# Optimization experiments

Hardware: AMD Instinct MI355X
Metric: run time of the kernel (lower is better)

Reference implementation:

```python
import jax, jax.numpy as jnp
import numpy as np

B_, N, C, H = 2048, 49, 384, 12
WH, WW = 7, 7
HEAD_DIM = C // H
SCALE = HEAD_DIM ** -0.5
TABLE = (2 * WH - 1) * (2 * WW - 1)  # 169


def _relative_position_index():
    coords = np.stack(np.meshgrid(np.arange(WH), np.arange(WW), indexing='ij'))  # [2,Wh,Ww]
    flat = coords.reshape(2, -1)  # [2,N]
    rel = flat[:, :, None] - flat[:, None, :]  # [2,N,N]
    rel = rel.transpose(1, 2, 0).astype(np.int32)  # [N,N,2]
    rel[:, :, 0] += WH - 1
    rel[:, :, 1] += WW - 1
    rel[:, :, 0] *= 2 * WW - 1
    return rel.sum(-1)  # [N,N] int32 in [0,169)


def setup_inputs() -> dict:
    key = jax.random.key(0)
    ks = jax.random.split(key, 8)
    return {
        'x': jax.random.normal(ks[0], (B_, N, C), jnp.float32),
        'mask': jax.random.normal(ks[1], (B_, 1, N, N), jnp.float32),
        'stagein': jax.random.uniform(ks[2], (B_, N, C), jnp.float32),
        'rel_bias_table': jax.random.normal(ks[3], (TABLE, H), jnp.float32) * 0.02,
        'rel_pos_index': jnp.asarray(_relative_position_index()),
        'qkv_w': jax.random.normal(ks[4], (3 * C, C), jnp.float32) * 0.02,
        'qkv_b': jax.random.normal(ks[5], (3 * C,), jnp.float32) * 0.02,
        'proj_w': jax.random.normal(ks[6], (C, C), jnp.float32) * 0.02,
        'proj_b': jax.random.normal(ks[7], (C,), jnp.float32) * 0.02,
    }


def reference(x, mask, stagein, rel_bias_table, rel_pos_index, qkv_w, qkv_b, proj_w, proj_b):
    x = x * stagein  # stagein is not None branch
    qkv = x @ qkv_w.T + qkv_b  # [B_, N, 3C]
    qkv = qkv.reshape(B_, N, 3, H, HEAD_DIM).transpose(2, 0, 3, 1, 4)  # [3,B_,H,N,hd]
    q, k, v = qkv[0], qkv[1], qkv[2]
    q = q * SCALE
    attn = jnp.einsum('bhnd,bhmd->bhnm', q, k)  # [B_,H,N,N]
    # relative position bias gather: [N*N] -> [N,N,H] -> [1,H,N,N]
    bias = rel_bias_table[rel_pos_index.reshape(-1)].reshape(N, N, H)
    bias = bias.transpose(2, 0, 1)[None]
    attn = jax.nn.softmax(attn + bias + mask, axis=-1)
    out = jnp.einsum('bhnm,bhmd->bhnd', attn, v)  # [B_,H,N,hd]
    out = out.transpose(0, 2, 1, 3).reshape(B_, N, C)
    return out @ proj_w.T + proj_b
```

## Files before the change

kernel.cpp:

```cpp
#include <hip/hip_runtime.h>
#include <hip/hip_bf16.h>
#include <stdint.h>

#define NWIN 2048
#define NTOK 49
#define CDIM 384
#define NHEAD 12
#define HD 32
#define C3 1152
#define NN2 2401
#define MROWS 100352

typedef __bf16 bf16x8 __attribute__((ext_vector_type(8)));
typedef float f32x4 __attribute__((ext_vector_type(4)));
typedef uint32_t u32x4 __attribute__((ext_vector_type(4)));
typedef unsigned int u32;

static __device__ __forceinline__ unsigned short f2bf(float f) {
  uint32_t u = __builtin_bit_cast(uint32_t, f);
  u += 0x7fffu + ((u >> 16) & 1u);
  return (unsigned short)(u >> 16);
}

static __device__ __forceinline__ u32 pk2(float a, float b) {
  return (u32)f2bf(a) | ((u32)f2bf(b) << 16);
}

static __device__ __forceinline__ void gload_lds16(const void* g, void* l) {
  __builtin_amdgcn_global_load_lds((const __attribute__((address_space(1))) void*)g,
                                   (__attribute__((address_space(3))) void*)l,
                                   16, 0, 0);
}

static __device__ __forceinline__ bf16x8 zero8() {
  u32x4 z = {0u, 0u, 0u, 0u};
  return __builtin_bit_cast(bf16x8, z);
}

__global__ void prep_kernel(const float* __restrict__ qkv_w, const float* __restrict__ proj_w,
                            const float* __restrict__ table, const int* __restrict__ idx,
                            unsigned short* __restrict__ wq, unsigned short* __restrict__ wp,
                            float* __restrict__ biasT) {
  const int NW1 = C3 * CDIM;
  const int NW2 = CDIM * CDIM;
  const int NB = NHEAD * NN2;
  int i = blockIdx.x * blockDim.x + threadIdx.x;
  int stride = gridDim.x * blockDim.x;
  for (int t = i; t < NW1 + NW2 + NB; t += stride) {
    if (t < NW1) {
      wq[t] = f2bf(qkv_w[t]);
    } else if (t < NW1 + NW2) {
      int j = t - NW1;
      wp[j] = f2bf(proj_w[j]);
    } else {
      int j = t - NW1 - NW2;
      int h = j / NN2;
      int nm = j - h * NN2;
      int m = nm / 49, n = nm - m * 49;
      biasT[j] = table[idx[n * 49 + m] * NHEAD + h];
    }
  }
}

__global__ void maskT_kernel(const float* __restrict__ mask, float* __restrict__ maskT) {
  __shared__ float t[NN2];
  const int b = blockIdx.x;
  for (int i = threadIdx.x; i < NN2; i += 256) t[i] = mask[(size_t)b * NN2 + i];
  __syncthreads();
  for (int i = threadIdx.x; i < NN2; i += 256) {
    int m = i / 49, n = i - m * 49;
    maskT[(size_t)b * NN2 + i] = t[n * 49 + m];
  }
}

__global__ void mul_kernel(const float4* __restrict__ x, const float4* __restrict__ s,
                           u32x4* __restrict__ A, int n8) {
  int i0 = blockIdx.x * blockDim.x + threadIdx.x;
  int stride = gridDim.x * blockDim.x;
  for (int t = i0; t < n8; t += stride) {
    float4 a0 = x[2 * t], a1 = x[2 * t + 1];
    float4 b0 = s[2 * t], b1 = s[2 * t + 1];
    union { unsigned short us[8]; u32x4 v; } o;
    o.us[0] = f2bf(a0.x * b0.x); o.us[1] = f2bf(a0.y * b0.y);
    o.us[2] = f2bf(a0.z * b0.z); o.us[3] = f2bf(a0.w * b0.w);
    o.us[4] = f2bf(a1.x * b1.x); o.us[5] = f2bf(a1.y * b1.y);
    o.us[6] = f2bf(a1.z * b1.z); o.us[7] = f2bf(a1.w * b1.w);
    A[t] = o.v;
  }
}

__launch_bounds__(512, 2)
__global__ void qkv_gemm(const unsigned short* __restrict__ A,
                         const unsigned short* __restrict__ Bw,
                         const float* __restrict__ qkvb,
                         unsigned short* __restrict__ qo,
                         unsigned short* __restrict__ ko,
                         unsigned short* __restrict__ vo) {
  __shared__ unsigned short As[128 * 64];
  __shared__ unsigned short Bs[128 * 64];
  const int tid = threadIdx.x;
  const int w = tid >> 6, l = tid & 63;
  const int l15 = l & 15, lhi = l >> 4;
  const int wgid = (blockIdx.x & 7) * 882 + (blockIdx.x >> 3);
  const int mt = wgid / 9, nt = wgid - mt * 9;
  const int wr = w >> 2, wc = w & 3;
  const int srow = tid >> 3;
  const int scb = (tid & 7) ^ (srow & 7);
  const unsigned short* Ag = A + (size_t)(mt * 128 + srow) * CDIM + scb * 8;
  const unsigned short* Bg = Bw + (size_t)(nt * 128 + srow) * CDIM + scb * 8;
  unsigned short* Asl = As + srow * 64 + (tid & 7) * 8;
  unsigned short* Bsl = Bs + srow * 64 + (tid & 7) * 8;
  const f32x4 z4 = {0.f, 0.f, 0.f, 0.f};
  f32x4 acc[4][2];
#pragma unroll
  for (int m = 0; m < 4; ++m)
#pragma unroll
    for (int n = 0; n < 2; ++n) acc[m][n] = z4;
  const int xr = l15 & 7;
  for (int kt = 0; kt < 6; ++kt) {
    const unsigned short* ag = Ag + kt * 64;
    const unsigned short* bg = Bg + kt * 64;
    gload_lds16(ag, Asl);
    gload_lds16(ag + 64 * CDIM, Asl + 4096);
    gload_lds16(bg, Bsl);
    gload_lds16(bg + 64 * CDIM, Bsl + 4096);
    __syncthreads();
#pragma unroll
    for (int kk = 0; kk < 2; ++kk) {
      const int sl = ((kk << 2) | lhi) ^ xr;
      bf16x8 af[4], bfr[2];
#pragma unroll
      for (int m = 0; m < 4; ++m)
        af[m] = *(const bf16x8*)(As + (wr * 64 + m * 16 + l15) * 64 + sl * 8);
#pragma unroll
      for (int n = 0; n < 2; ++n)
        bfr[n] = *(const bf16x8*)(Bs + (wc * 32 + n * 16 + l15) * 64 + sl * 8);
#pragma unroll
      for (int m = 0; m < 4; ++m)
#pragma unroll
        for (int n = 0; n < 2; ++n)
          acc[m][n] = __builtin_amdgcn_mfma_f32_16x16x32_bf16(af[m], bfr[n], acc[m][n], 0, 0, 0);
    }
    __syncthreads();
  }
  const float SCALE_F = 0.17677669529663687f;
  const int six = nt * 4 + wc;
  const int which = six / 12;
  const int cbase = (six - which * 12) * 32;
  unsigned short* outw = (which == 0) ? qo : ((which == 1) ? ko : vo);
  const float* bptr = qkvb + which * CDIM;
  float bv2[2];
#pragma unroll
  for (int n = 0; n < 2; ++n) bv2[n] = bptr[cbase + n * 16 + l15];
#pragma unroll
  for (int m = 0; m < 4; ++m) {
    const int r0 = mt * 128 + wr * 64 + m * 16 + lhi * 4;
#pragma unroll
    for (int j = 0; j < 4; ++j) {
      unsigned short* orow = outw + (size_t)(r0 + j) * CDIM;
#pragma unroll
      for (int n = 0; n < 2; ++n) {
        float val = acc[m][n][j] + bv2[n];
        if (which == 0) val *= SCALE_F;
        orow[cbase + n * 16 + l15] = f2bf(val);
      }
    }
  }
}

__launch_bounds__(256, 2)
__global__ void attn_kernel(const unsigned short* __restrict__ q,
                            const unsigned short* __restrict__ kmat,
                            const unsigned short* __restrict__ vmat,
                            const float* __restrict__ maskT,
                            const float* __restrict__ biasT,
                            unsigned short* __restrict__ attnout) {
  __shared__ unsigned short vT_lds[4][32 * 72];
  const int tid = threadIdx.x;
  const int w = tid >> 6, l = tid & 63;
  const int l15 = l & 15, lhi = l >> 4;
  const int wg = (blockIdx.x & 7) * 768 + (blockIdx.x >> 3);
  const int b = wg / 3, it = wg - b * 3;
  unsigned short* Vw = &vT_lds[w][0];
  const float* maskb = maskT + (size_t)b * NN2;
  const f32x4 z4 = {0.f, 0.f, 0.f, 0.f};
  const int h = it * 4 + w;
  const size_t rowbase = (size_t)b * NTOK * CDIM + h * HD;
  const unsigned short* qb = q + rowbase;
  const unsigned short* kb = kmat + rowbase;
  const unsigned short* vb = vmat + rowbase;
  {
    const int n = l;
    unsigned short tmp[32];
    if (n < 49) {
      *(u32x4*)(&tmp[0])  = *(const u32x4*)(vb + (size_t)n * CDIM);
      *(u32x4*)(&tmp[8])  = *(const u32x4*)(vb + (size_t)n * CDIM + 8);
      *(u32x4*)(&tmp[16]) = *(const u32x4*)(vb + (size_t)n * CDIM + 16);
      *(u32x4*)(&tmp[24]) = *(const u32x4*)(vb + (size_t)n * CDIM + 24);
    } else {
#pragma unroll
      for (int d2 = 0; d2 < 32; ++d2) tmp[d2] = 0;
    }
#pragma unroll
    for (int d2 = 0; d2 < 32; ++d2) Vw[d2 * 72 + n] = tmp[d2];
  }
  bf16x8 aq[4], bk[4];
#pragma unroll
  for (int t = 0; t < 4; ++t) {
    const int row = t * 16 + l15;
    if (row < 49) {
      aq[t] = *(const bf16x8*)(qb + (size_t)row * CDIM + lhi * 8);
      bk[t] = *(const bf16x8*)(kb + (size_t)row * CDIM + lhi * 8);
    } else {
      aq[t] = zero8();
      bk[t] = zero8();
    }
  }
  const float* biash = biasT + h * NN2;
  u32 P4[4][4][2];
#pragma unroll
  for (int nt = 0; nt < 4; ++nt) {
    f32x4 s4[4];
#pragma unroll
    for (int mt = 0; mt < 4; ++mt)
      s4[mt] = __builtin_amdgcn_mfma_f32_16x16x32_bf16(bk[mt], aq[nt], z4, 0, 0, 0);
    const int n = nt * 16 + l15;
#pragma unroll
    for (int mt = 0; mt < 4; ++mt) {
#pragma unroll
      for (int r = 0; r < 4; ++r) {
        const int m = mt * 16 + lhi * 4 + r;
        float val = -1e30f;
        if (n < 49 && m < 49)
          val = s4[mt][r] + biash[m * 49 + n] + maskb[m * 49 + n];
        s4[mt][r] = val;
      }
    }
    float mx = s4[0][0];
#pragma unroll
    for (int mt = 0; mt < 4; ++mt)
#pragma unroll
      for (int r = 0; r < 4; ++r) mx = fmaxf(mx, s4[mt][r]);
    mx = fmaxf(mx, __shfl_xor(mx, 16));
    mx = fmaxf(mx, __shfl_xor(mx, 32));
    float sum = 0.f;
#pragma unroll
    for (int mt = 0; mt < 4; ++mt)
#pragma unroll
      for (int r = 0; r < 4; ++r) {
        s4[mt][r] = __expf(s4[mt][r] - mx);
        sum += s4[mt][r];
      }
    sum += __shfl_xor(sum, 16);
    sum += __shfl_xor(sum, 32);
    const float rinv = 1.0f / sum;
#pragma unroll
    for (int mt = 0; mt < 4; ++mt) {
      P4[nt][mt][0] = pk2(s4[mt][0] * rinv, s4[mt][1] * rinv);
      P4[nt][mt][1] = pk2(s4[mt][2] * rinv, s4[mt][3] * rinv);
    }
  }
  const int sA = ((l >> 4) & 1) * 32 + l15;
  const int sB = sA + 16;
  const bool hi_sel = (l & 32) != 0;
  f32x4 o[4][2];
#pragma unroll
  for (int ti = 0; ti < 4; ++ti) { o[ti][0] = z4; o[ti][1] = z4; }
#pragma unroll
  for (int kk = 0; kk < 2; ++kk) {
    bf16x8 bv0 = *(const bf16x8*)(Vw + l15 * 72 + kk * 32 + lhi * 8);
    bf16x8 bv1 = *(const bf16x8*)(Vw + (16 + l15) * 72 + kk * 32 + lhi * 8);
#pragma unroll
    for (int ti = 0; ti < 4; ++ti) {
      int x0 = __shfl((int)P4[ti][2 * kk][0], sA);
      int x1 = __shfl((int)P4[ti][2 * kk][1], sA);
      int y0 = __shfl((int)P4[ti][2 * kk + 1][0], sA);
      int y1 = __shfl((int)P4[ti][2 * kk + 1][1], sA);
      int x2 = __shfl((int)P4[ti][2 * kk][0], sB);
      int x3 = __shfl((int)P4[ti][2 * kk][1], sB);
      int y2 = __shfl((int)P4[ti][2 * kk + 1][0], sB);
      int y3 = __shfl((int)P4[ti][2 * kk + 1][1], sB);
      u32x4 f;
      f[0] = (u32)(hi_sel ? y0 : x0);
      f[1] = (u32)(hi_sel ? y1 : x1);
      f[2] = (u32)(hi_sel ? y2 : x2);
      f[3] = (u32)(hi_sel ? y3 : x3);
      bf16x8 pa = __builtin_bit_cast(bf16x8, f);
      o[ti][0] = __builtin_amdgcn_mfma_f32_16x16x32_bf16(pa, bv0, o[ti][0], 0, 0, 0);
      o[ti][1] = __builtin_amdgcn_mfma_f32_16x16x32_bf16(pa, bv1, o[ti][1], 0, 0, 0);
    }
  }
#pragma unroll
  for (int ti = 0; ti < 4; ++ti) {
#pragma unroll
    for (int r = 0; r < 4; ++r) {
      const int n = ti * 16 + lhi * 4 + r;
      if (n < 49) {
        unsigned short* orow = attnout + ((size_t)b * NTOK + n) * CDIM + h * HD;
        orow[l15] = f2bf(o[ti][0][r]);
        orow[16 + l15] = f2bf(o[ti][1][r]);
      }
    }
  }
}

__launch_bounds__(512, 2)
__global__ void proj_gemm(const unsigned short* __restrict__ A,
                          const unsigned short* __restrict__ Bw,
                          const float* __restrict__ pb,
                          float* __restrict__ out) {
  __shared__ unsigned short As[128 * 64];
  __shared__ unsigned short Bs[128 * 64];
  const int tid = threadIdx.x;
  const int w = tid >> 6, l = tid & 63;
  const int l15 = l & 15, lhi = l >> 4;
  const int wgid = (blockIdx.x & 7) * 294 + (blockIdx.x >> 3);
  const int mt = wgid / 3, nt = wgid - mt * 3;
  const int wr = w >> 2, wc = w & 3;
  const int srow = tid >> 3;
  const int scb = (tid & 7) ^ (srow & 7);
  const unsigned short* Ag = A + (size_t)(mt * 128 + srow) * CDIM + scb * 8;
  const unsigned short* Bg = Bw + (size_t)(nt * 128 + srow) * CDIM + scb * 8;
  unsigned short* Asl = As + srow * 64 + (tid & 7) * 8;
  unsigned short* Bsl = Bs + srow * 64 + (tid & 7) * 8;
  const f32x4 z4 = {0.f, 0.f, 0.f, 0.f};
  f32x4 acc[4][2];
#pragma unroll
  for (int m = 0; m < 4; ++m)
#pragma unroll
    for (int n = 0; n < 2; ++n) acc[m][n] = z4;
  const int xr = l15 & 7;
  for (int kt = 0; kt < 6; ++kt) {
    const unsigned short* ag = Ag + kt * 64;
    const unsigned short* bg = Bg + kt * 64;
    gload_lds16(ag, Asl);
    gload_lds16(ag + 64 * CDIM, Asl + 4096);
    gload_lds16(bg, Bsl);
    gload_lds16(bg + 64 * CDIM, Bsl + 4096);
    __syncthreads();
#pragma unroll
    for (int kk = 0; kk < 2; ++kk) {
      const int sl = ((kk << 2) | lhi) ^ xr;
      bf16x8 af[4], bfr[2];
#pragma unroll
      for (int m = 0; m < 4; ++m)
        af[m] = *(const bf16x8*)(As + (wr * 64 + m * 16 + l15) * 64 + sl * 8);
#pragma unroll
      for (int n = 0; n < 2; ++n)
        bfr[n] = *(const bf16x8*)(Bs + (wc * 32 + n * 16 + l15) * 64 + sl * 8);
#pragma unroll
      for (int m = 0; m < 4; ++m)
#pragma unroll
        for (int n = 0; n < 2; ++n)
          acc[m][n] = __builtin_amdgcn_mfma_f32_16x16x32_bf16(af[m], bfr[n], acc[m][n], 0, 0, 0);
    }
    __syncthreads();
  }
#pragma unroll
  for (int m = 0; m < 4; ++m) {
    const int r0 = mt * 128 + wr * 64 + m * 16 + lhi * 4;
#pragma unroll
    for (int j = 0; j < 4; ++j) {
      float* orow = out + (size_t)(r0 + j) * CDIM;
#pragma unroll
      for (int n = 0; n < 2; ++n) {
        const int c = nt * 128 + wc * 32 + n * 16 + l15;
        orow[c] = acc[m][n][j] + pb[c];
      }
    }
  }
}

extern "C" void kernel_launch(void* const* d_in, const int* in_sizes, int n_in,
                              void* d_out, int out_size, void* d_ws, size_t ws_size,
                              hipStream_t stream) {
  const float* x       = (const float*)d_in[0];
  const float* mask    = (const float*)d_in[1];
  const float* stagein = (const float*)d_in[2];
  const float* table   = (const float*)d_in[3];
  const int*   idx     = (const int*)d_in[4];
  const float* qkv_w   = (const float*)d_in[5];
  const float* qkv_b   = (const float*)d_in[6];
  const float* proj_w  = (const float*)d_in[7];
  const float* proj_b  = (const float*)d_in[8];
  float* out = (float*)d_out;
  char* ws = (char*)d_ws;

  const size_t SZA = (size_t)MROWS * CDIM * 2;
  unsigned short* Abf = (unsigned short*)(ws);
  unsigned short* qb  = (unsigned short*)(ws + SZA);
  unsigned short* kb  = (unsigned short*)(ws + 2 * SZA);
  unsigned short* vb  = (unsigned short*)(ws + 3 * SZA);
  unsigned short* wq  = (unsigned short*)(ws + 4 * SZA);
  unsigned short* wp  = (unsigned short*)(ws + 4 * SZA + (size_t)C3 * CDIM * 2);
  float* biasT        = (float*)(ws + 4 * SZA + (size_t)C3 * CDIM * 2 + (size_t)CDIM * CDIM * 2);
  float* maskT        = biasT + (size_t)NHEAD * NN2;
  unsigned short* attnout = Abf;

  prep_kernel<<<dim3(512), dim3(256), 0, stream>>>(qkv_w, proj_w, table, idx, wq, wp, biasT);
  maskT_kernel<<<dim3(NWIN), dim3(256), 0, stream>>>(mask, maskT);
  mul_kernel<<<dim3(2048), dim3(256), 0, stream>>>((const float4*)x, (const float4*)stagein,
                                                   (u32x4*)Abf, MROWS * CDIM / 8);
  qkv_gemm<<<dim3(784 * 9), dim3(512), 0, stream>>>(Abf, wq, qkv_b, qb, kb, vb);
  attn_kernel<<<dim3(NWIN * 3), dim3(256), 0, stream>>>(qb, kb, vb, maskT, biasT, attnout);
  proj_gemm<<<dim3(784 * 3), dim3(512), 0, stream>>>(attnout, wp, proj_b, out);
}
```

Measured before the change: 419.6 us.

## Fuse stagein multiply into QKV GEMM and double-buffer LDS tiles

Removes the separate elementwise kernel that multiplied x by stagein and wrote a bf16 copy. The QKV GEMM now loads fp32 x and stagein directly, multiplies, converts to bf16 and writes into swizzled LDS. It also double-buffers A and B in LDS so the next k-tile's loads overlap with the current MFMA work. The cost is that each of the 9 N-tiles per M row re-reads fp32 x and stagein, which is four times the bytes of the old bf16 A, and LDS use per block doubles, which may hurt occupancy.

Result: slower. 523.3 us (+24.7%).

```diff
diff --git a/kernel.cpp b/kernel.cpp
--- a/kernel.cpp
+++ b/kernel.cpp
@@ -73,43 +73,33 @@
   }
 }
 
-__global__ void mul_kernel(const float4* __restrict__ x, const float4* __restrict__ s,
-                           u32x4* __restrict__ A, int n8) {
-  int i0 = blockIdx.x * blockDim.x + threadIdx.x;
-  int stride = gridDim.x * blockDim.x;
-  for (int t = i0; t < n8; t += stride) {
-    float4 a0 = x[2 * t], a1 = x[2 * t + 1];
-    float4 b0 = s[2 * t], b1 = s[2 * t + 1];
-    union { unsigned short us[8]; u32x4 v; } o;
-    o.us[0] = f2bf(a0.x * b0.x); o.us[1] = f2bf(a0.y * b0.y);
-    o.us[2] = f2bf(a0.z * b0.z); o.us[3] = f2bf(a0.w * b0.w);
-    o.us[4] = f2bf(a1.x * b1.x); o.us[5] = f2bf(a1.y * b1.y);
-    o.us[6] = f2bf(a1.z * b1.z); o.us[7] = f2bf(a1.w * b1.w);
-    A[t] = o.v;
-  }
-}
-
 __launch_bounds__(512, 2)
-__global__ void qkv_gemm(const unsigned short* __restrict__ A,
+__global__ void qkv_gemm(const float* __restrict__ x,
+                         const float* __restrict__ stg,
                          const unsigned short* __restrict__ Bw,
                          const float* __restrict__ qkvb,
                          unsigned short* __restrict__ qo,
                          unsigned short* __restrict__ ko,
                          unsigned short* __restrict__ vo) {
-  __shared__ unsigned short As[128 * 64];
-  __shared__ unsigned short Bs[128 * 64];
+  __shared__ unsigned short Alds[2][128 * 64];
+  __shared__ unsigned short Blds[2][128 * 64];
   const int tid = threadIdx.x;
   const int w = tid >> 6, l = tid & 63;
   const int l15 = l & 15, lhi = l >> 4;
   const int wgid = (blockIdx.x & 7) * 882 + (blockIdx.x >> 3);
   const int mt = wgid / 9, nt = wgid - mt * 9;
   const int wr = w >> 2, wc = w & 3;
+  const int arow = tid >> 2;
+  const int ac4 = tid & 3;
+  const float* xg = x   + (size_t)(mt * 128 + arow) * CDIM + ac4 * 16;
+  const float* sg = stg + (size_t)(mt * 128 + arow) * CDIM + ac4 * 16;
+  const int cb0 = (2 * ac4) ^ (arow & 7);
+  const int cb1 = (2 * ac4 + 1) ^ (arow & 7);
+  unsigned short* Aw0 = &Alds[0][0] + arow * 64;
   const int srow = tid >> 3;
   const int scb = (tid & 7) ^ (srow & 7);
-  const unsigned short* Ag = A + (size_t)(mt * 128 + srow) * CDIM + scb * 8;
   const unsigned short* Bg = Bw + (size_t)(nt * 128 + srow) * CDIM + scb * 8;
-  unsigned short* Asl = As + srow * 64 + (tid & 7) * 8;
-  unsigned short* Bsl = Bs + srow * 64 + (tid & 7) * 8;
+  unsigned short* Bsl = &Blds[0][0] + srow * 64 + (tid & 7) * 8;
   const f32x4 z4 = {0.f, 0.f, 0.f, 0.f};
   f32x4 acc[4][2];
 #pragma unroll
@@ -117,31 +107,74 @@
 #pragma unroll
     for (int n = 0; n < 2; ++n) acc[m][n] = z4;
   const int xr = l15 & 7;
+  float4 xv[4], sv[4];
+  {
+    const float4* xp = (const float4*)xg;
+    const float4* sp = (const float4*)sg;
+#pragma unroll
+    for (int i = 0; i < 4; ++i) { xv[i] = xp[i]; sv[i] = sp[i]; }
+    gload_lds16(Bg, Bsl);
+    gload_lds16(Bg + 64 * CDIM, Bsl + 4096);
+    u32x4 o0, o1;
+    o0[0] = pk2(xv[0].x * sv[0].x, xv[0].y * sv[0].y);
+    o0[1] = pk2(xv[0].z * sv[0].z, xv[0].w * sv[0].w);
+    o0[2] = pk2(xv[1].x * sv[1].x, xv[1].y * sv[1].y);
+    o0[3] = pk2(xv[1].z * sv[1].z, xv[1].w * sv[1].w);
+    o1[0] = pk2(xv[2].x * sv[2].x, xv[2].y * sv[2].y);
+    o1[1] = pk2(xv[2].z * sv[2].z, xv[2].w * sv[2].w);
+    o1[2] = pk2(xv[3].x * sv[3].x, xv[3].y * sv[3].y);
+    o1[3] = pk2(xv[3].z * sv[3].z, xv[3].w * sv[3].w);
+    *(u32x4*)(Aw0 + cb0 * 8) = o0;
+    *(u32x4*)(Aw0 + cb1 * 8) = o1;
+    __syncthreads();
+  }
+  int cur = 0;
   for (int kt = 0; kt < 6; ++kt) {
-    const unsigned short* ag = Ag + kt * 64;
-    const unsigned short* bg = Bg + kt * 64;
-    gload_lds16(ag, Asl);
-    gload_lds16(ag + 64 * CDIM, Asl + 4096);
-    gload_lds16(bg, Bsl);
-    gload_lds16(bg + 64 * CDIM, Bsl + 4096);
-    __syncthreads();
+    const bool pf = (kt < 5);
+    if (pf) {
+      const unsigned short* bg = Bg + (kt + 1) * 64;
+      unsigned short* bd = Bsl + (cur ^ 1) * 8192;
+      gload_lds16(bg, bd);
+      gload_lds16(bg + 64 * CDIM, bd + 4096);
+      const float4* xp = (const float4*)(xg + (kt + 1) * 64);
+      const float4* sp = (const float4*)(sg + (kt + 1) * 64);
+#pragma unroll
+      for (int i = 0; i < 4; ++i) { xv[i] = xp[i]; sv[i] = sp[i]; }
+    }
+    const unsigned short* Ard = &Alds[0][0] + cur * 8192;
+    const unsigned short* Brd = &Blds[0][0] + cur * 8192;
 #pragma unroll
     for (int kk = 0; kk < 2; ++kk) {
       const int sl = ((kk << 2) | lhi) ^ xr;
       bf16x8 af[4], bfr[2];
 #pragma unroll
       for (int m = 0; m < 4; ++m)
-        af[m] = *(const bf16x8*)(As + (wr * 64 + m * 16 + l15) * 64 + sl * 8);
+        af[m] = *(const bf16x8*)(Ard + (wr * 64 + m * 16 + l15) * 64 + sl * 8);
 #pragma unroll
       for (int n = 0; n < 2; ++n)
-        bfr[n] = *(const bf16x8*)(Bs + (wc * 32 + n * 16 + l15) * 64 + sl * 8);
+        bfr[n] = *(const bf16x8*)(Brd + (wc * 32 + n * 16 + l15) * 64 + sl * 8);
 #pragma unroll
       for (int m = 0; m < 4; ++m)
 #pragma unroll
         for (int n = 0; n < 2; ++n)
           acc[m][n] = __builtin_amdgcn_mfma_f32_16x16x32_bf16(af[m], bfr[n], acc[m][n], 0, 0, 0);
     }
-    __syncthreads();
+    if (pf) {
+      u32x4 o0, o1;
+      o0[0] = pk2(xv[0].x * sv[0].x, xv[0].y * sv[0].y);
+      o0[1] = pk2(xv[0].z * sv[0].z, xv[0].w * sv[0].w);
+      o0[2] = pk2(xv[1].x * sv[1].x, xv[1].y * sv[1].y);
+      o0[3] = pk2(xv[1].z * sv[1].z, xv[1].w * sv[1].w);
+      o1[0] = pk2(xv[2].x * sv[2].x, xv[2].y * sv[2].y);
+      o1[1] = pk2(xv[2].z * sv[2].z, xv[2].w * sv[2].w);
+      o1[2] = pk2(xv[3].x * sv[3].x, xv[3].y * sv[3].y);
+      o1[3] = pk2(xv[3].z * sv[3].z, xv[3].w * sv[3].w);
+      unsigned short* aw = Aw0 + (cur ^ 1) * 8192;
+      *(u32x4*)(aw + cb0 * 8) = o0;
+      *(u32x4*)(aw + cb1 * 8) = o1;
+      __syncthreads();
+      cur ^= 1;
+    }
   }
   const float SCALE_F = 0.17677669529663687f;
   const int six = nt * 4 + wc;
@@ -387,7 +420,7 @@
   char* ws = (char*)d_ws;
 
   const size_t SZA = (size_t)MROWS * CDIM * 2;
-  unsigned short* Abf = (unsigned short*)(ws);
+  unsigned short* attnout = (unsigned short*)(ws);
   unsigned short* qb  = (unsigned short*)(ws + SZA);
   unsigned short* kb  = (unsigned short*)(ws + 2 * SZA);
   unsigned short* vb  = (unsigned short*)(ws + 3 * SZA);
@@ -395,13 +428,10 @@
   unsigned short* wp  = (unsigned short*)(ws + 4 * SZA + (size_t)C3 * CDIM * 2);
   float* biasT        = (float*)(ws + 4 * SZA + (size_t)C3 * CDIM * 2 + (size_t)CDIM * CDIM * 2);
   float* maskT        = biasT + (size_t)NHEAD * NN2;
-  unsigned short* attnout = Abf;
 
   prep_kernel<<<dim3(512), dim3(256), 0, stream>>>(qkv_w, proj_w, table, idx, wq, wp, biasT);
   maskT_kernel<<<dim3(NWIN), dim3(256), 0, stream>>>(mask, maskT);
-  mul_kernel<<<dim3(2048), dim3(256), 0, stream>>>((const float4*)x, (const float4*)stagein,
-                                                   (u32x4*)Abf, MROWS * CDIM / 8);
-  qkv_gemm<<<dim3(784 * 9), dim3(512), 0, stream>>>(Abf, wq, qkv_b, qb, kb, vb);
+  qkv_gemm<<<dim3(784 * 9), dim3(512), 0, stream>>>(x, stagein, wq, qkv_b, qb, kb, vb);
   attn_kernel<<<dim3(NWIN * 3), dim3(256), 0, stream>>>(qb, kb, vb, maskT, biasT, attnout);
   proj_gemm<<<dim3(784 * 3), dim3(512), 0, stream>>>(attnout, wp, proj_b, out);
 }
```
